# Performance work log

Measured on AMD Instinct MI355X. Metric: run time of the kernel, lower is better.

The kernel has to match this reference:

```python
import jax, jax.numpy as jnp
import numpy as np

K = 15000  # TCPR top-k

def _norm(x):
    # torch F.normalize(p=2, dim=-1, eps=1e-12)
    return x / jnp.maximum(jnp.linalg.norm(x, axis=-1, keepdims=True), 1e-12)

def setup_inputs() -> dict:
    key = jax.random.key(0)
    k1, k2, k3 = jax.random.split(key, 3)
    features = jax.random.normal(k1, (8, 1024, 1024), dtype=jnp.float32)
    base_features = jax.random.normal(k2, (100000, 1024), dtype=jnp.float32)
    support_labels = jax.random.randint(k3, (8, 128), 0, 64)
    return {"features": features, "base_features": base_features, "support_labels": support_labels}

def reference(features, base_features, support_labels):
    # features: [E, N, D]; base_features: [B, D]; support_labels: [E, S] (only width used)
    features = _norm(features)
    n_support = support_labels.shape[1]
    support = features[:, :n_support]                      # [E, S, D]
    base = _norm(base_features)                            # [B, D]
    support_mean = jnp.mean(support, axis=1)               # [E, D]
    sim = _norm(support_mean) @ base.T                     # [E, B] cosine sims
    sim_cos, pred = jax.lax.top_k(sim, K)                  # [E, K]
    w = jnp.sqrt(sim_cos)
    w = w / jnp.sum(w, axis=1, keepdims=True)              # [E, K]
    approx = jnp.einsum('ek,ekd->ed', w, base[pred])       # weighted gather-sum -> [E, D]
    approx = _norm(approx)[:, None, :]                     # [E, 1, D]
    # get_cos_sin (sin unused downstream)
    cos_val = (jnp.sum(features * approx, axis=-1, keepdims=True)
               / jnp.linalg.norm(features, axis=-1, keepdims=True)
               / jnp.linalg.norm(approx, axis=-1, keepdims=True))
    # remove projection onto base approximation, renormalize
    return _norm(features - cos_val * approx)
```

## Files before the change

### kernel.cpp

```cpp
#include <hip/hip_runtime.h>
#include <math.h>

#define NBASE 100000
#define DIM   1024
#define NE    8
#define NSUP  128
#define KSEL  15000
#define NB1   4096
#define CAP2  1024

__device__ __forceinline__ float dot4(float4 a, float4 b) {
    return a.x*b.x + a.y*b.y + a.z*b.z + a.w*b.w;
}
__device__ __forceinline__ float4 scale4(float4 a, float s) {
    return make_float4(a.x*s, a.y*s, a.z*s, a.w*s);
}
__device__ __forceinline__ float4 add4(float4 a, float4 b) {
    return make_float4(a.x+b.x, a.y+b.y, a.z+b.z, a.w+b.w);
}
__device__ __forceinline__ float wave_sum_xor(float v) {
    #pragma unroll
    for (int m = 1; m < 64; m <<= 1) v += __shfl_xor(v, m, 64);
    return v;
}
__device__ __forceinline__ float wave_sum(float v) {
    #pragma unroll
    for (int off = 32; off > 0; off >>= 1) v += __shfl_down(v, off, 64);
    return v;
}
__device__ __forceinline__ float block_sum(float v, float* red) {
    int lane = threadIdx.x & 63, wv = threadIdx.x >> 6;
    v = wave_sum(v);
    __syncthreads();
    if (lane == 0) red[wv] = v;
    __syncthreads();
    return red[0] + red[1] + red[2] + red[3];
}
__device__ __forceinline__ int bin1(float s) {
    int b = (int)((s + 1.0001f) * ((float)NB1 / 2.0002f));
    return min(max(b, 0), NB1 - 1);
}
__device__ __forceinline__ int bin2(float s, int B) {
    float lo2 = -1.0001f + (float)B * (2.0002f / (float)NB1);
    int b = (int)((s - lo2) * ((float)NB1 / 2.0002f * 256.0f));
    return min(max(b, 0), 255);
}

__global__ void k1a(const float* __restrict__ F, float* __restrict__ Qpart) {
    int blk = blockIdx.x;
    int e = blk >> 5, g = blk & 31;
    int wv = threadIdx.x >> 6, lane = threadIdx.x & 63;
    int r = g * 4 + wv;
    const float4* row = (const float4*)(F + ((size_t)e * 1024 + r) * DIM);
    float4 f0 = row[lane], f1 = row[64+lane], f2 = row[128+lane], f3 = row[192+lane];
    float ss = dot4(f0,f0) + dot4(f1,f1) + dot4(f2,f2) + dot4(f3,f3);
    ss = wave_sum_xor(ss);
    float inv = 1.f / fmaxf(sqrtf(ss), 1e-12f);
    __shared__ float part[4][1024];
    float4* p4 = (float4*)part[wv];
    p4[lane]     = scale4(f0, inv);
    p4[64+lane]  = scale4(f1, inv);
    p4[128+lane] = scale4(f2, inv);
    p4[192+lane] = scale4(f3, inv);
    __syncthreads();
    int tid = threadIdx.x;
    const float4* pp = (const float4*)part;
    float4 s = add4(add4(pp[tid], pp[256+tid]), add4(pp[512+tid], pp[768+tid]));
    ((float4*)Qpart)[(size_t)(e*32+g)*256 + tid] = s;
}

__global__ void k1b(const float* __restrict__ Qpart, float* __restrict__ Q) {
    int e = blockIdx.x, tid = threadIdx.x;
    __shared__ float red[4];
    const float4* qp = (const float4*)Qpart;
    float4 s = make_float4(0.f,0.f,0.f,0.f);
    #pragma unroll 4
    for (int g = 0; g < 32; ++g) s = add4(s, qp[(size_t)(e*32+g)*256 + tid]);
    float ss = block_sum(dot4(s,s), red);
    float inv = 1.f / fmaxf(sqrtf(ss), 1e-12f);
    ((float4*)Q)[e*256 + tid] = scale4(s, inv);
}

__global__ void k2_sim(const float* __restrict__ Bse, const float* __restrict__ Q,
                       float* __restrict__ S, float* __restrict__ ST,
                       float* __restrict__ InvN) {
    __shared__ float q_sh[NE * DIM];
    int tid = threadIdx.x, wv = tid >> 6, lane = tid & 63;
    {
        const float4* Q4 = (const float4*)Q;
        float4* q4 = (float4*)q_sh;
        #pragma unroll
        for (int k = 0; k < 8; ++k) q4[k*256 + tid] = Q4[k*256 + tid];
    }
    __syncthreads();
    const float4* q4 = (const float4*)q_sh;
    size_t i = (size_t)blockIdx.x * 4 + wv;
    const float4* b4 = (const float4*)(Bse + i * DIM);
    float4 b0 = b4[lane], b1 = b4[64+lane], b2 = b4[128+lane], b3 = b4[192+lane];
    float pv[9];
    pv[8] = dot4(b0,b0) + dot4(b1,b1) + dot4(b2,b2) + dot4(b3,b3);
    #pragma unroll
    for (int e = 0; e < NE; ++e) {
        float4 q0 = q4[e*256+lane],     q1 = q4[e*256+64+lane];
        float4 q2 = q4[e*256+128+lane], q3 = q4[e*256+192+lane];
        pv[e] = dot4(b0,q0) + dot4(b1,q1) + dot4(b2,q2) + dot4(b3,q3);
    }
    #pragma unroll
    for (int v = 0; v < 9; ++v) pv[v] = wave_sum_xor(pv[v]);
    float invn = 1.f / fmaxf(sqrtf(pv[8]), 1e-12f);
    if (lane < 8) {
        float v = pv[0];
        #pragma unroll
        for (int e = 1; e < 8; ++e) v = (lane == e) ? pv[e] : v;
        float sv = v * invn;
        S[i*NE + lane] = sv;
        ST[(size_t)lane*NBASE + i] = sv;
    }
    if (lane == 0) InvN[i] = invn;
}

__global__ void k3a(const float* __restrict__ ST, int* __restrict__ Hist) {
    int e = blockIdx.x >> 5, chunk = blockIdx.x & 31;
    __shared__ int h[NB1];
    for (int b = threadIdx.x; b < NB1; b += 256) h[b] = 0;
    __syncthreads();
    const int per = (NBASE + 31) / 32;
    int i0 = chunk * per, i1 = min(i0 + per, NBASE);
    for (int i = i0 + threadIdx.x; i < i1; i += 256) {
        float s = ST[(size_t)e*NBASE + i];
        atomicAdd(&h[bin1(s)], 1);
    }
    __syncthreads();
    for (int b = threadIdx.x; b < NB1; b += 256)
        if (h[b]) atomicAdd(&Hist[e*NB1 + b], h[b]);
}

__global__ void k3b(const int* __restrict__ Hist, int* __restrict__ Meta) {
    int e = blockIdx.x, tid = threadIdx.x;
    __shared__ int gsum[256];
    int s = 0;
    #pragma unroll
    for (int j = 0; j < 16; ++j) s += Hist[e*NB1 + tid*16 + j];
    gsum[tid] = s;
    __syncthreads();
    if (tid == 0) {
        int cum = 0;
        for (int g = 255; g >= 0; --g) {
            if (cum + gsum[g] >= KSEL) {
                for (int b = g*16 + 15;; --b) {
                    int c = Hist[e*NB1 + b];
                    if (cum + c >= KSEL) { Meta[e*4+0] = b; Meta[e*4+1] = KSEL - cum; break; }
                    cum += c;
                }
                break;
            }
            cum += gsum[g];
        }
    }
}

__global__ void k3c(const float* __restrict__ ST, const int* __restrict__ Meta,
                    int* __restrict__ SubHist) {
    int e = blockIdx.x >> 5, chunk = blockIdx.x & 31;
    int B = Meta[e*4];
    __shared__ int h[256];
    h[threadIdx.x] = 0;
    __syncthreads();
    const int per = (NBASE + 31) / 32;
    int i0 = chunk * per, i1 = min(i0 + per, NBASE);
    for (int i = i0 + threadIdx.x; i < i1; i += 256) {
        float s = ST[(size_t)e*NBASE + i];
        if (bin1(s) == B) atomicAdd(&h[bin2(s, B)], 1);
    }
    __syncthreads();
    if (h[threadIdx.x]) atomicAdd(&SubHist[e*256 + threadIdx.x], h[threadIdx.x]);
}

__global__ void k3d(const int* __restrict__ SubHist, int* __restrict__ Meta) {
    int e = blockIdx.x;
    if (threadIdx.x != 0) return;
    int need1 = Meta[e*4+1], cum = 0;
    for (int b = 255; b >= 0; --b) {
        int c = SubHist[e*256 + b];
        if (cum + c >= need1) { Meta[e*4+2] = b; Meta[e*4+3] = need1 - cum; return; }
        cum += c;
    }
    Meta[e*4+2] = 0; Meta[e*4+3] = need1 - cum;
}

__global__ void k3e(const float* __restrict__ S, const int* __restrict__ Meta,
                    unsigned char* __restrict__ Flags, int* __restrict__ CandI,
                    float* __restrict__ CandV, int* __restrict__ CandCnt) {
    int i = blockIdx.x * 256 + threadIdx.x;
    if (i >= NBASE) return;
    const float4* S4 = (const float4*)S;
    float4 sa = S4[(size_t)i*2], sb = S4[(size_t)i*2 + 1];
    float sv[8] = {sa.x, sa.y, sa.z, sa.w, sb.x, sb.y, sb.z, sb.w};
    unsigned long long flw = 0ull;
    #pragma unroll
    for (int e = 0; e < 8; ++e) {
        int B = Meta[e*4], B2 = Meta[e*4+2];
        int b = bin1(sv[e]);
        int fl = 0;
        if (b > B) fl = 1;
        else if (b == B) {
            int b2 = bin2(sv[e], B);
            if (b2 > B2) fl = 1;
            else if (b2 == B2) {
                int k = atomicAdd(&CandCnt[e], 1);
                if (k < CAP2) { CandI[e*CAP2 + k] = i; CandV[e*CAP2 + k] = sv[e]; }
            }
        }
        flw |= ((unsigned long long)fl) << (8*e);
    }
    *(unsigned long long*)(Flags + (size_t)i * 8) = flw;
}

__global__ void k3f(const int* __restrict__ Meta, const int* __restrict__ CandCnt,
                    int* __restrict__ CandI, const float* __restrict__ CandV,
                    unsigned char* __restrict__ Flags) {
    int e = blockIdx.x;
    if (threadIdx.x != 0) return;
    int need2 = Meta[e*4+3];
    int n = min(CandCnt[e], CAP2);
    for (int t = 0; t < need2; ++t) {
        int best = -1, bi = 0; float bv = 0.f;
        for (int j = 0; j < n; ++j) {
            int ij = CandI[e*CAP2 + j];
            if (ij < 0) continue;
            float vj = CandV[e*CAP2 + j];
            if (best < 0 || vj > bv || (vj == bv && ij < bi)) { best = j; bv = vj; bi = ij; }
        }
        if (best < 0) break;
        Flags[(size_t)bi * NE + e] = 1;
        CandI[e*CAP2 + best] = -1;
    }
}

__global__ void k4_part(const float* __restrict__ Bse, const float* __restrict__ S,
                        const float* __restrict__ InvN, const unsigned char* __restrict__ Flags,
                        float* __restrict__ Part) {
    int tid = threadIdx.x;
    float acc[NE][4];
    #pragma unroll
    for (int e = 0; e < NE; ++e)
        #pragma unroll
        for (int j = 0; j < 4; ++j) acc[e][j] = 0.f;
    for (int i = blockIdx.x; i < NBASE; i += gridDim.x) {
        unsigned long long fl = *(const unsigned long long*)(Flags + (size_t)i * 8);
        if (!fl) continue;
        float inv = InvN[i];
        const float4* S4 = (const float4*)S;
        float4 sa = S4[(size_t)i*2], sb = S4[(size_t)i*2 + 1];
        float sv[8] = {sa.x, sa.y, sa.z, sa.w, sb.x, sb.y, sb.z, sb.w};
        float coef[NE];
        #pragma unroll
        for (int e = 0; e < NE; ++e)
            coef[e] = ((fl >> (8*e)) & 0xffull) ? sqrtf(fmaxf(sv[e], 0.f)) * inv : 0.f;
        float4 b = ((const float4*)(Bse + (size_t)i * DIM))[tid];
        #pragma unroll
        for (int e = 0; e < NE; ++e) {
            acc[e][0] += coef[e] * b.x;
            acc[e][1] += coef[e] * b.y;
            acc[e][2] += coef[e] * b.z;
            acc[e][3] += coef[e] * b.w;
        }
    }
    float4* P4 = (float4*)Part;
    #pragma unroll
    for (int e = 0; e < NE; ++e)
        P4[(size_t)blockIdx.x*2048 + e*256 + tid] =
            make_float4(acc[e][0], acc[e][1], acc[e][2], acc[e][3]);
}

__global__ void k4_atomic(const float* __restrict__ Bse, const float* __restrict__ S,
                          const float* __restrict__ InvN, const unsigned char* __restrict__ Flags,
                          float* __restrict__ Acc) {
    int tid = threadIdx.x;
    float acc[NE][4];
    #pragma unroll
    for (int e = 0; e < NE; ++e)
        #pragma unroll
        for (int j = 0; j < 4; ++j) acc[e][j] = 0.f;
    for (int i = blockIdx.x; i < NBASE; i += gridDim.x) {
        unsigned long long fl = *(const unsigned long long*)(Flags + (size_t)i * 8);
        if (!fl) continue;
        float inv = InvN[i];
        const float4* S4 = (const float4*)S;
        float4 sa = S4[(size_t)i*2], sb = S4[(size_t)i*2 + 1];
        float sv[8] = {sa.x, sa.y, sa.z, sa.w, sb.x, sb.y, sb.z, sb.w};
        float coef[NE];
        #pragma unroll
        for (int e = 0; e < NE; ++e)
            coef[e] = ((fl >> (8*e)) & 0xffull) ? sqrtf(fmaxf(sv[e], 0.f)) * inv : 0.f;
        float4 b = ((const float4*)(Bse + (size_t)i * DIM))[tid];
        #pragma unroll
        for (int e = 0; e < NE; ++e) {
            acc[e][0] += coef[e] * b.x;
            acc[e][1] += coef[e] * b.y;
            acc[e][2] += coef[e] * b.z;
            acc[e][3] += coef[e] * b.w;
        }
    }
    #pragma unroll
    for (int e = 0; e < NE; ++e)
        #pragma unroll
        for (int j = 0; j < 4; ++j)
            atomicAdd(&Acc[e*DIM + tid*4 + j], acc[e][j]);
}

__global__ void k4b(const float* __restrict__ Part, float* __restrict__ Acc, int nparts) {
    int g = blockIdx.x * 256 + threadIdx.x;
    int c = g & 2047, s = g >> 11;
    const float4* P4 = (const float4*)Part;
    float4 a = make_float4(0.f,0.f,0.f,0.f);
    for (int b = s; b < nparts; b += 16) a = add4(a, P4[(size_t)b*2048 + c]);
    atomicAdd(&Acc[c*4+0], a.x);
    atomicAdd(&Acc[c*4+1], a.y);
    atomicAdd(&Acc[c*4+2], a.z);
    atomicAdd(&Acc[c*4+3], a.w);
}

__global__ void k5(const float* __restrict__ Acc, float* __restrict__ A) {
    int e = blockIdx.x, tid = threadIdx.x;
    __shared__ float red[4];
    float4 a = ((const float4*)Acc)[e*256 + tid];
    float ss = block_sum(dot4(a,a), red);
    float inv = 1.f / fmaxf(sqrtf(ss), 1e-12f);
    ((float4*)A)[e*256 + tid] = scale4(a, inv);
}

__global__ void k6(const float* __restrict__ F, const float* __restrict__ A,
                   float* __restrict__ Out) {
    int wv = threadIdx.x >> 6, lane = threadIdx.x & 63;
    size_t rid = (size_t)blockIdx.x * 4 + wv;
    int e = (int)(rid >> 10);
    const float4* f4 = (const float4*)(F + rid * DIM);
    const float4* a4 = (const float4*)(A + (size_t)e * DIM);
    float4 f0 = f4[lane], f1 = f4[64+lane], f2 = f4[128+lane], f3 = f4[192+lane];
    float4 a0 = a4[lane], a1 = a4[64+lane], a2 = a4[128+lane], a3 = a4[192+lane];
    float ss = dot4(f0,f0) + dot4(f1,f1) + dot4(f2,f2) + dot4(f3,f3);
    ss = wave_sum_xor(ss);
    float invf = 1.f / fmaxf(sqrtf(ss), 1e-12f);
    f0 = scale4(f0, invf); f1 = scale4(f1, invf); f2 = scale4(f2, invf); f3 = scale4(f3, invf);
    float c = dot4(f0,a0) + dot4(f1,a1) + dot4(f2,a2) + dot4(f3,a3);
    c = wave_sum_xor(c);
    float4 r0 = make_float4(f0.x - c*a0.x, f0.y - c*a0.y, f0.z - c*a0.z, f0.w - c*a0.w);
    float4 r1 = make_float4(f1.x - c*a1.x, f1.y - c*a1.y, f1.z - c*a1.z, f1.w - c*a1.w);
    float4 r2 = make_float4(f2.x - c*a2.x, f2.y - c*a2.y, f2.z - c*a2.z, f2.w - c*a2.w);
    float4 r3 = make_float4(f3.x - c*a3.x, f3.y - c*a3.y, f3.z - c*a3.z, f3.w - c*a3.w);
    float rs = dot4(r0,r0) + dot4(r1,r1) + dot4(r2,r2) + dot4(r3,r3);
    rs = wave_sum_xor(rs);
    float invr = 1.f / fmaxf(sqrtf(rs), 1e-12f);
    float4* o4 = (float4*)(Out + rid * DIM);
    o4[lane]     = scale4(r0, invr);
    o4[64+lane]  = scale4(r1, invr);
    o4[128+lane] = scale4(r2, invr);
    o4[192+lane] = scale4(r3, invr);
}

extern "C" void kernel_launch(void* const* d_in, const int* in_sizes, int n_in,
                              void* d_out, int out_size, void* d_ws, size_t ws_size,
                              hipStream_t stream) {
    const float* F   = (const float*)d_in[0];
    const float* Bse = (const float*)d_in[1];
    float* Out = (float*)d_out;

    char* ws = (char*)d_ws;
    size_t off = 0;
    auto alloc = [&](size_t bytes) -> void* {
        void* p = ws + off;
        off += (bytes + 255) & ~(size_t)255;
        return p;
    };
    float* Q     = (float*)alloc((size_t)NE * DIM * 4);
    float* Qpart = (float*)alloc((size_t)NE * 32 * DIM * 4);
    float* S     = (float*)alloc((size_t)NBASE * NE * 4);
    float* ST    = (float*)alloc((size_t)NE * NBASE * 4);
    float* InvN  = (float*)alloc((size_t)NBASE * 4);
    unsigned char* Flags = (unsigned char*)alloc((size_t)NBASE * NE);
    int*   Zero  = (int*)alloc((size_t)(NE*NB1 + NE*256 + NE) * 4);
    int*   Hist    = Zero;
    int*   SubHist = Zero + NE*NB1;
    int*   CandCnt = Zero + NE*NB1 + NE*256;
    int*   Meta  = (int*)alloc((size_t)NE * 4 * 4);
    int*   CandI = (int*)alloc((size_t)NE * CAP2 * 4);
    float* CandV = (float*)alloc((size_t)NE * CAP2 * 4);
    float* Acc   = (float*)alloc((size_t)NE * DIM * 4);
    float* A     = (float*)alloc((size_t)NE * DIM * 4);

    int nparts = 0;
    float* Part = nullptr;
    size_t partBytes512 = (size_t)512 * NE * DIM * 4;
    size_t partBytes256 = (size_t)256 * NE * DIM * 4;
    if (ws_size >= off + partBytes512)      { nparts = 512; Part = (float*)alloc(partBytes512); }
    else if (ws_size >= off + partBytes256) { nparts = 256; Part = (float*)alloc(partBytes256); }

    hipMemsetAsync(Zero, 0, (size_t)(NE*NB1 + NE*256 + NE) * 4, stream);
    hipMemsetAsync(Acc, 0, (size_t)NE * DIM * 4, stream);

    k1a<<<NE*32, 256, 0, stream>>>(F, Qpart);
    k1b<<<NE, 256, 0, stream>>>(Qpart, Q);
    k2_sim<<<(NBASE+3)/4, 256, 0, stream>>>(Bse, Q, S, ST, InvN);
    k3a<<<NE*32, 256, 0, stream>>>(ST, Hist);
    k3b<<<NE, 256, 0, stream>>>(Hist, Meta);
    k3c<<<NE*32, 256, 0, stream>>>(ST, Meta, SubHist);
    k3d<<<NE, 64, 0, stream>>>(SubHist, Meta);
    k3e<<<(NBASE+255)/256, 256, 0, stream>>>(S, Meta, Flags, CandI, CandV, CandCnt);
    k3f<<<NE, 64, 0, stream>>>(Meta, CandCnt, CandI, CandV, Flags);
    if (nparts) {
        k4_part<<<nparts, 256, 0, stream>>>(Bse, S, InvN, Flags, Part);
        k4b<<<128, 256, 0, stream>>>(Part, Acc, nparts);
    } else {
        k4_atomic<<<512, 256, 0, stream>>>(Bse, S, InvN, Flags, Acc);
    }
    k5<<<NE, 256, 0, stream>>>(Acc, A);
    k6<<<(NE*1024)/4, 256, 0, stream>>>(F, A, Out);
}
```

Measured before the change: 882.2 us.

## Compact selected base rows into an index list before the weighted gather-sum

Adds a stream-compaction kernel that uses wave ballots to write the indices and per-episode coefficients of all flagged base rows into dense arrays. The gather-sum kernels then walk only that list, prefetching the next index, instead of scanning all 100000 flag words with divergent skips. It also raises the number of partial-sum blocks up to 2048 when the workspace allows and widens the reduction grid to match. The cost is an extra kernel launch, unordered atomic slot assignment that changes summation order, and a larger partial buffer to reduce.

```diff
diff --git a/kernel.cpp b/kernel.cpp
--- a/kernel.cpp
+++ b/kernel.cpp
@@ -237,34 +237,69 @@
     }
 }
 
-__global__ void k4_part(const float* __restrict__ Bse, const float* __restrict__ S,
-                        const float* __restrict__ InvN, const unsigned char* __restrict__ Flags,
-                        float* __restrict__ Part) {
-    int tid = threadIdx.x;
-    float acc[NE][4];
-    #pragma unroll
-    for (int e = 0; e < NE; ++e)
-        #pragma unroll
-        for (int j = 0; j < 4; ++j) acc[e][j] = 0.f;
-    for (int i = blockIdx.x; i < NBASE; i += gridDim.x) {
-        unsigned long long fl = *(const unsigned long long*)(Flags + (size_t)i * 8);
-        if (!fl) continue;
+__global__ void k3g(const float* __restrict__ S, const float* __restrict__ InvN,
+                    const unsigned char* __restrict__ Flags,
+                    int* __restrict__ SelIdx, float* __restrict__ Coef,
+                    int* __restrict__ SelCnt) {
+    int i = blockIdx.x * 256 + threadIdx.x;
+    int lane = threadIdx.x & 63;
+    unsigned long long fl = 0ull;
+    bool act = false;
+    if (i < NBASE) {
+        fl = *(const unsigned long long*)(Flags + (size_t)i * 8);
+        act = (fl != 0ull);
+    }
+    unsigned long long ball = __ballot(act);
+    int total = __popcll(ball);
+    int prefix = __popcll(ball & ((1ull << lane) - 1ull));
+    int base = 0;
+    if (lane == 0 && total) base = atomicAdd(SelCnt, total);
+    base = __shfl(base, 0, 64);
+    if (act) {
+        int slot = base + prefix;
+        SelIdx[slot] = i;
         float inv = InvN[i];
         const float4* S4 = (const float4*)S;
         float4 sa = S4[(size_t)i*2], sb = S4[(size_t)i*2 + 1];
         float sv[8] = {sa.x, sa.y, sa.z, sa.w, sb.x, sb.y, sb.z, sb.w};
-        float coef[NE];
-        #pragma unroll
-        for (int e = 0; e < NE; ++e)
-            coef[e] = ((fl >> (8*e)) & 0xffull) ? sqrtf(fmaxf(sv[e], 0.f)) * inv : 0.f;
-        float4 b = ((const float4*)(Bse + (size_t)i * DIM))[tid];
+        float cf[8];
+        #pragma unroll
+        for (int e = 0; e < 8; ++e)
+            cf[e] = ((fl >> (8*e)) & 0xffull) ? sqrtf(fmaxf(sv[e], 0.f)) * inv : 0.f;
+        float4* C4 = (float4*)(Coef + (size_t)slot * 8);
+        C4[0] = make_float4(cf[0], cf[1], cf[2], cf[3]);
+        C4[1] = make_float4(cf[4], cf[5], cf[6], cf[7]);
+    }
+}
+
+__global__ void k4_part(const float* __restrict__ Bse, const int* __restrict__ SelIdx,
+                        const float* __restrict__ Coef, const int* __restrict__ SelCnt,
+                        float* __restrict__ Part) {
+    int tid = threadIdx.x;
+    int n = *SelCnt;
+    int G = gridDim.x;
+    float acc[NE][4];
+    #pragma unroll
+    for (int e = 0; e < NE; ++e)
+        #pragma unroll
+        for (int j = 0; j < 4; ++j) acc[e][j] = 0.f;
+    int j = blockIdx.x;
+    int idx = (j < n) ? SelIdx[j] : 0;
+    for (; j < n; j += G) {
+        int jn = j + G;
+        int nidx = (jn < n) ? SelIdx[jn] : 0;
+        const float4* cf4 = (const float4*)(Coef + (size_t)j * 8);
+        float4 c0 = cf4[0], c1 = cf4[1];
+        float cf[8] = {c0.x, c0.y, c0.z, c0.w, c1.x, c1.y, c1.z, c1.w};
+        float4 b = ((const float4*)(Bse + (size_t)idx * DIM))[tid];
         #pragma unroll
         for (int e = 0; e < NE; ++e) {
-            acc[e][0] += coef[e] * b.x;
-            acc[e][1] += coef[e] * b.y;
-            acc[e][2] += coef[e] * b.z;
-            acc[e][3] += coef[e] * b.w;
-        }
+            acc[e][0] += cf[e] * b.x;
+            acc[e][1] += cf[e] * b.y;
+            acc[e][2] += cf[e] * b.z;
+            acc[e][3] += cf[e] * b.w;
+        }
+        idx = nidx;
     }
     float4* P4 = (float4*)Part;
     #pragma unroll
@@ -273,40 +308,40 @@
             make_float4(acc[e][0], acc[e][1], acc[e][2], acc[e][3]);
 }
 
-__global__ void k4_atomic(const float* __restrict__ Bse, const float* __restrict__ S,
-                          const float* __restrict__ InvN, const unsigned char* __restrict__ Flags,
+__global__ void k4_atomic(const float* __restrict__ Bse, const int* __restrict__ SelIdx,
+                          const float* __restrict__ Coef, const int* __restrict__ SelCnt,
                           float* __restrict__ Acc) {
     int tid = threadIdx.x;
+    int n = *SelCnt;
+    int G = gridDim.x;
     float acc[NE][4];
     #pragma unroll
     for (int e = 0; e < NE; ++e)
         #pragma unroll
         for (int j = 0; j < 4; ++j) acc[e][j] = 0.f;
-    for (int i = blockIdx.x; i < NBASE; i += gridDim.x) {
-        unsigned long long fl = *(const unsigned long long*)(Flags + (size_t)i * 8);
-        if (!fl) continue;
-        float inv = InvN[i];
-        const float4* S4 = (const float4*)S;
-        float4 sa = S4[(size_t)i*2], sb = S4[(size_t)i*2 + 1];
-        float sv[8] = {sa.x, sa.y, sa.z, sa.w, sb.x, sb.y, sb.z, sb.w};
-        float coef[NE];
-        #pragma unroll
-        for (int e = 0; e < NE; ++e)
-            coef[e] = ((fl >> (8*e)) & 0xffull) ? sqrtf(fmaxf(sv[e], 0.f)) * inv : 0.f;
-        float4 b = ((const float4*)(Bse + (size_t)i * DIM))[tid];
+    int j = blockIdx.x;
+    int idx = (j < n) ? SelIdx[j] : 0;
+    for (; j < n; j += G) {
+        int jn = j + G;
+        int nidx = (jn < n) ? SelIdx[jn] : 0;
+        const float4* cf4 = (const float4*)(Coef + (size_t)j * 8);
+        float4 c0 = cf4[0], c1 = cf4[1];
+        float cf[8] = {c0.x, c0.y, c0.z, c0.w, c1.x, c1.y, c1.z, c1.w};
+        float4 b = ((const float4*)(Bse + (size_t)idx * DIM))[tid];
         #pragma unroll
         for (int e = 0; e < NE; ++e) {
-            acc[e][0] += coef[e] * b.x;
-            acc[e][1] += coef[e] * b.y;
-            acc[e][2] += coef[e] * b.z;
-            acc[e][3] += coef[e] * b.w;
-        }
+            acc[e][0] += cf[e] * b.x;
+            acc[e][1] += cf[e] * b.y;
+            acc[e][2] += cf[e] * b.z;
+            acc[e][3] += cf[e] * b.w;
+        }
+        idx = nidx;
     }
     #pragma unroll
     for (int e = 0; e < NE; ++e)
         #pragma unroll
-        for (int j = 0; j < 4; ++j)
-            atomicAdd(&Acc[e*DIM + tid*4 + j], acc[e][j]);
+        for (int q = 0; q < 4; ++q)
+            atomicAdd(&Acc[e*DIM + tid*4 + q], acc[e][q]);
 }
 
 __global__ void k4b(const float* __restrict__ Part, float* __restrict__ Acc, int nparts) {
@@ -314,7 +349,7 @@
     int c = g & 2047, s = g >> 11;
     const float4* P4 = (const float4*)Part;
     float4 a = make_float4(0.f,0.f,0.f,0.f);
-    for (int b = s; b < nparts; b += 16) a = add4(a, P4[(size_t)b*2048 + c]);
+    for (int b = s; b < nparts; b += 32) a = add4(a, P4[(size_t)b*2048 + c]);
     atomicAdd(&Acc[c*4+0], a.x);
     atomicAdd(&Acc[c*4+1], a.y);
     atomicAdd(&Acc[c*4+2], a.z);
@@ -379,24 +414,31 @@
     float* ST    = (float*)alloc((size_t)NE * NBASE * 4);
     float* InvN  = (float*)alloc((size_t)NBASE * 4);
     unsigned char* Flags = (unsigned char*)alloc((size_t)NBASE * NE);
-    int*   Zero  = (int*)alloc((size_t)(NE*NB1 + NE*256 + NE) * 4);
+    int*   Zero  = (int*)alloc((size_t)(NE*NB1 + NE*256 + NE + 1) * 4);
     int*   Hist    = Zero;
     int*   SubHist = Zero + NE*NB1;
     int*   CandCnt = Zero + NE*NB1 + NE*256;
+    int*   SelCnt  = Zero + NE*NB1 + NE*256 + NE;
     int*   Meta  = (int*)alloc((size_t)NE * 4 * 4);
     int*   CandI = (int*)alloc((size_t)NE * CAP2 * 4);
     float* CandV = (float*)alloc((size_t)NE * CAP2 * 4);
     float* Acc   = (float*)alloc((size_t)NE * DIM * 4);
     float* A     = (float*)alloc((size_t)NE * DIM * 4);
+    int*   SelIdx = (int*)alloc((size_t)NBASE * 4);
+    float* Coef   = (float*)alloc((size_t)NBASE * 8 * 4);
 
     int nparts = 0;
     float* Part = nullptr;
-    size_t partBytes512 = (size_t)512 * NE * DIM * 4;
-    size_t partBytes256 = (size_t)256 * NE * DIM * 4;
-    if (ws_size >= off + partBytes512)      { nparts = 512; Part = (float*)alloc(partBytes512); }
-    else if (ws_size >= off + partBytes256) { nparts = 256; Part = (float*)alloc(partBytes256); }
-
-    hipMemsetAsync(Zero, 0, (size_t)(NE*NB1 + NE*256 + NE) * 4, stream);
+    size_t perPart = (size_t)NE * DIM * 4;
+    for (int cand : {2048, 1024, 512, 256}) {
+        if (ws_size >= off + (size_t)cand * perPart) {
+            nparts = cand;
+            Part = (float*)alloc((size_t)cand * perPart);
+            break;
+        }
+    }
+
+    hipMemsetAsync(Zero, 0, (size_t)(NE*NB1 + NE*256 + NE + 1) * 4, stream);
     hipMemsetAsync(Acc, 0, (size_t)NE * DIM * 4, stream);
 
     k1a<<<NE*32, 256, 0, stream>>>(F, Qpart);
@@ -408,11 +450,12 @@
     k3d<<<NE, 64, 0, stream>>>(SubHist, Meta);
     k3e<<<(NBASE+255)/256, 256, 0, stream>>>(S, Meta, Flags, CandI, CandV, CandCnt);
     k3f<<<NE, 64, 0, stream>>>(Meta, CandCnt, CandI, CandV, Flags);
+    k3g<<<(NBASE+255)/256, 256, 0, stream>>>(S, InvN, Flags, SelIdx, Coef, SelCnt);
     if (nparts) {
-        k4_part<<<nparts, 256, 0, stream>>>(Bse, S, InvN, Flags, Part);
-        k4b<<<128, 256, 0, stream>>>(Part, Acc, nparts);
+        k4_part<<<nparts, 256, 0, stream>>>(Bse, SelIdx, Coef, SelCnt, Part);
+        k4b<<<256, 256, 0, stream>>>(Part, Acc, nparts);
     } else {
-        k4_atomic<<<512, 256, 0, stream>>>(Bse, S, InvN, Flags, Acc);
+        k4_atomic<<<512, 256, 0, stream>>>(Bse, SelIdx, Coef, SelCnt, Acc);
     }
     k5<<<NE, 256, 0, stream>>>(Acc, A);
     k6<<<(NE*1024)/4, 256, 0, stream>>>(F, A, Out);
```

Measured after the change: 732.1 us. 17.0% less time.
